# Kernel optimization log

Measured on AMD Instinct MI355X. Metric: run time of the kernel, lower is better.

Reference implementation:

```python
import jax, jax.numpy as jnp
import numpy as np

N_NODES = 100000
N_EDGES = 3200000
N_SAMPLES = 8
EPS_CONST = 1e-8


def setup_inputs() -> dict:
    key = jax.random.key(0)
    k1, k2, k3, k4 = jax.random.split(key, 4)
    mu = jax.random.normal(k1, (N_NODES,), dtype=jnp.float32)
    log_sigma = jax.random.normal(k2, (N_NODES,), dtype=jnp.float32)
    eps = jax.random.normal(k3, (N_SAMPLES, N_NODES), dtype=jnp.float32)
    edges = jax.random.randint(k4, (N_EDGES, 2), 0, N_NODES, dtype=jnp.int64)
    return {"mu": mu, "log_sigma": log_sigma, "eps": eps, "edges": edges, "n_samples": N_SAMPLES}


def reference(mu, log_sigma, eps, edges, n_samples):
    # c_samples: [S, N]
    c = mu + jnp.exp(log_sigma) * eps
    ci = c[:, edges[:, 0]]  # [S, E] gather
    cj = c[:, edges[:, 1]]  # [S, E] gather
    p = jax.nn.sigmoid(ci * cj)
    # original: sum over edges of mean over samples
    loglik = jnp.log(p + EPS_CONST).mean(axis=0).sum()
    return loglik
```

## Files before the change

### kernel.cpp

```cpp
#include <hip/hip_runtime.h>
#include <hip/hip_fp16.h>


__global__ void compute_c_h8(const float* __restrict__ mu,
                             const float* __restrict__ ls,
                             const float* __restrict__ eps,
                             __half2* __restrict__ c, int N,
                             const unsigned int* __restrict__ raw_edges,
                             int* __restrict__ flag,
                             float* __restrict__ out, int out_size) {
    if (blockIdx.x == gridDim.x - 1) {
        int lane = threadIdx.x;
        if (lane < 64) {
            unsigned int acc = 0;
#pragma unroll
            for (int k = 0; k < 4; ++k) acc |= raw_edges[2 * (lane * 4 + k) + 1];
#pragma unroll
            for (int off = 32; off > 0; off >>= 1) acc |= __shfl_down(acc, off, 64);
            if (lane == 0) *flag = (acc == 0u) ? 1 : 0;
        }
        for (int i = threadIdx.x; i < out_size; i += blockDim.x) out[i] = 0.0f;
        return;
    }
    int n = blockIdx.x * blockDim.x + threadIdx.x;
    if (n >= N) return;
    float m  = mu[n];
    float sg = __expf(ls[n]);
    float v[8];
#pragma unroll
    for (int s = 0; s < 8; ++s) v[s] = m + sg * eps[(size_t)s * N + n];
    __half2* dst = c + (size_t)n * 4;
#pragma unroll
    for (int s = 0; s < 4; ++s) dst[s] = __floats2half2_rn(v[2 * s], v[2 * s + 1]);
}

__global__ void compute_c_gen(const float* __restrict__ mu,
                              const float* __restrict__ ls,
                              const float* __restrict__ eps,
                              __half* __restrict__ c, int N, int S,
                              const unsigned int* __restrict__ raw_edges,
                              int* __restrict__ flag,
                              float* __restrict__ out, int out_size) {
    if (blockIdx.x == gridDim.x - 1) {
        int lane = threadIdx.x;
        if (lane < 64) {
            unsigned int acc = 0;
#pragma unroll
            for (int k = 0; k < 4; ++k) acc |= raw_edges[2 * (lane * 4 + k) + 1];
#pragma unroll
            for (int off = 32; off > 0; off >>= 1) acc |= __shfl_down(acc, off, 64);
            if (lane == 0) *flag = (acc == 0u) ? 1 : 0;
        }
        for (int i = threadIdx.x; i < out_size; i += blockDim.x) out[i] = 0.0f;
        return;
    }
    int n = blockIdx.x * blockDim.x + threadIdx.x;
    if (n >= N) return;
    float m  = mu[n];
    float sg = __expf(ls[n]);
    for (int s = 0; s < S; ++s) c[(size_t)n * S + s] = __float2half(m + sg * eps[(size_t)s * N + n]);
}

__device__ __forceinline__ float edge_term(uint4 A, uint4 B) {
    const __half2* ah = (const __half2*)&A;
    const __half2* bh = (const __half2*)&B;
    float t[8];
#pragma unroll
    for (int k = 0; k < 4; ++k) {
        __half2 xh = __hmul2(ah[k], bh[k]);
        float2 xf = __half22float2(xh);
        t[2 * k]     = fminf(__expf(-xf.x), 1.0e8f);
        t[2 * k + 1] = fminf(__expf(-xf.y), 1.0e8f);
    }
    float p0 = 1.0f + t[0];
    p0 = __builtin_fmaf(p0, t[1], p0);
    p0 = __builtin_fmaf(p0, t[2], p0);
    p0 = __builtin_fmaf(p0, t[3], p0);
    float p1 = 1.0f + t[4];
    p1 = __builtin_fmaf(p1, t[5], p1);
    p1 = __builtin_fmaf(p1, t[6], p1);
    p1 = __builtin_fmaf(p1, t[7], p1);
    return __logf(p0) + __logf(p1);
}

__global__ void __launch_bounds__(256, 8)
edge_loglik_s8(const void* __restrict__ edges_raw,
               const uint4* __restrict__ c,
               const int* __restrict__ flag,
               float* __restrict__ out,
               long long E, float inv_s) {
    long long tid    = (long long)blockIdx.x * blockDim.x + threadIdx.x;
    long long stride = (long long)gridDim.x * blockDim.x;
    float acc = 0.0f;
    bool is64 = (*flag != 0);

    if (!is64) {
        const int4* ep = (const int4*)edges_raw;
        long long P = E >> 1;
        for (long long q = tid; q < P; q += 2 * stride) {
            long long q1 = q + stride;
            bool has1 = q1 < P;
            int4 e0 = ep[q];
            int4 e1 = has1 ? ep[q1] : e0;
            uint4 a0 = c[e0.x], b0 = c[e0.y], d0 = c[e0.z], f0 = c[e0.w];
            uint4 a1 = c[e1.x], b1 = c[e1.y], d1 = c[e1.z], f1 = c[e1.w];
            float s = edge_term(a0, b0) + edge_term(d0, f0);
            if (has1) s += edge_term(a1, b1) + edge_term(d1, f1);
            acc += s;
        }
        if ((E & 1) && tid == 0) {
            const int2* el = (const int2*)edges_raw;
            int2 ij = el[E - 1];
            acc += edge_term(c[ij.x], c[ij.y]);
        }
    } else {
        const longlong2* ep = (const longlong2*)edges_raw;
        for (long long e = tid; e < E; e += stride) {
            longlong2 ij = ep[e];
            acc += edge_term(c[ij.x], c[ij.y]);
        }
    }

#pragma unroll
    for (int off = 32; off > 0; off >>= 1) acc += __shfl_down(acc, off, 64);
    __shared__ float wsum[8];
    int lane = threadIdx.x & 63;
    int wid  = threadIdx.x >> 6;
    if (lane == 0) wsum[wid] = acc;
    __syncthreads();
    if (threadIdx.x == 0) {
        float s = 0.0f;
        int nw = blockDim.x >> 6;
        for (int w = 0; w < nw; ++w) s += wsum[w];
        atomicAdd(out, -s * inv_s);
    }
}

__global__ void edge_loglik_gen(const void* __restrict__ edges_raw,
                                const __half* __restrict__ c,
                                const int* __restrict__ flag,
                                float* __restrict__ out,
                                long long E, int S, float inv_s) {
    long long tid    = (long long)blockIdx.x * blockDim.x + threadIdx.x;
    long long stride = (long long)gridDim.x * blockDim.x;
    float acc = 0.0f;
    bool is64 = (*flag != 0);
    for (long long e = tid; e < E; e += stride) {
        long long i, j;
        if (is64) {
            const long long* ed = (const long long*)edges_raw;
            i = ed[2 * e]; j = ed[2 * e + 1];
        } else {
            const int* ed = (const int*)edges_raw;
            i = ed[2 * e]; j = ed[2 * e + 1];
        }
        for (int s = 0; s < S; ++s) {
            float x = __half2float(c[i * S + s]) * __half2float(c[j * S + s]);
            acc += __logf(1.0f + fminf(__expf(-x), 1.0e8f));
        }
    }
#pragma unroll
    for (int off = 32; off > 0; off >>= 1) acc += __shfl_down(acc, off, 64);
    __shared__ float wsum[8];
    int lane = threadIdx.x & 63;
    int wid  = threadIdx.x >> 6;
    if (lane == 0) wsum[wid] = acc;
    __syncthreads();
    if (threadIdx.x == 0) {
        float s = 0.0f;
        int nw = blockDim.x >> 6;
        for (int w = 0; w < nw; ++w) s += wsum[w];
        atomicAdd(out, -s * inv_s);
    }
}

extern "C" void kernel_launch(void* const* d_in, const int* in_sizes, int n_in,
                              void* d_out, int out_size, void* d_ws, size_t ws_size,
                              hipStream_t stream) {
    const float* mu    = (const float*)d_in[0];
    const float* ls    = (const float*)d_in[1];
    const float* eps   = (const float*)d_in[2];
    const void*  edges = d_in[3];

    int       N = in_sizes[0];
    int       S = in_sizes[2] / N;
    long long E = (long long)in_sizes[3] / 2;

    __half* c   = (__half*)d_ws;
    int*   flag = (int*)((char*)d_ws + (size_t)N * S * sizeof(__half) + 256);
    float* out  = (float*)d_out;

    int cblocks = (N + 255) / 256 + 1;
    if (S == 8) {
        compute_c_h8<<<cblocks, 256, 0, stream>>>(mu, ls, eps, (__half2*)c, N,
                                                  (const unsigned int*)edges, flag, out, out_size);
        edge_loglik_s8<<<2048, 256, 0, stream>>>(edges, (const uint4*)c, flag, out, E, 1.0f / (float)S);
    } else {
        compute_c_gen<<<cblocks, 256, 0, stream>>>(mu, ls, eps, c, N, S,
                                                   (const unsigned int*)edges, flag, out, out_size);
        edge_loglik_gen<<<2048, 256, 0, stream>>>(edges, c, flag, out, E, S, 1.0f / (float)S);
    }
}
```

Baseline: 48.06 us.

## Bucket edges by node-block pairs and gather from shared-memory tiles

Adds a scatter pass that sorts edges into buckets keyed by pairs of 2048-node blocks. A compute pass then loads both node tiles into LDS and evaluates every edge in the bucket from shared memory. Overflow edges are handled by a few extra blocks, and the final reduction is done by the last block to finish. The goal is to replace random global gathers of the c table with LDS reads. The cost is an extra pass that reads all edges twice, plus record writes, global atomics and a third kernel launch. The edge format is now assumed to be int32 and the 64-bit detection flag is dropped.

```diff
diff --git a/kernel.cpp b/kernel.cpp
--- a/kernel.cpp
+++ b/kernel.cpp
@@ -2,64 +2,15 @@
 #include <hip/hip_fp16.h>
 
 
-__global__ void compute_c_h8(const float* __restrict__ mu,
-                             const float* __restrict__ ls,
-                             const float* __restrict__ eps,
-                             __half2* __restrict__ c, int N,
-                             const unsigned int* __restrict__ raw_edges,
-                             int* __restrict__ flag,
-                             float* __restrict__ out, int out_size) {
-    if (blockIdx.x == gridDim.x - 1) {
-        int lane = threadIdx.x;
-        if (lane < 64) {
-            unsigned int acc = 0;
-#pragma unroll
-            for (int k = 0; k < 4; ++k) acc |= raw_edges[2 * (lane * 4 + k) + 1];
-#pragma unroll
-            for (int off = 32; off > 0; off >>= 1) acc |= __shfl_down(acc, off, 64);
-            if (lane == 0) *flag = (acc == 0u) ? 1 : 0;
-        }
-        for (int i = threadIdx.x; i < out_size; i += blockDim.x) out[i] = 0.0f;
-        return;
-    }
-    int n = blockIdx.x * blockDim.x + threadIdx.x;
-    if (n >= N) return;
-    float m  = mu[n];
-    float sg = __expf(ls[n]);
-    float v[8];
-#pragma unroll
-    for (int s = 0; s < 8; ++s) v[s] = m + sg * eps[(size_t)s * N + n];
-    __half2* dst = c + (size_t)n * 4;
-#pragma unroll
-    for (int s = 0; s < 4; ++s) dst[s] = __floats2half2_rn(v[2 * s], v[2 * s + 1]);
-}
-
-__global__ void compute_c_gen(const float* __restrict__ mu,
-                              const float* __restrict__ ls,
-                              const float* __restrict__ eps,
-                              __half* __restrict__ c, int N, int S,
-                              const unsigned int* __restrict__ raw_edges,
-                              int* __restrict__ flag,
-                              float* __restrict__ out, int out_size) {
-    if (blockIdx.x == gridDim.x - 1) {
-        int lane = threadIdx.x;
-        if (lane < 64) {
-            unsigned int acc = 0;
-#pragma unroll
-            for (int k = 0; k < 4; ++k) acc |= raw_edges[2 * (lane * 4 + k) + 1];
-#pragma unroll
-            for (int off = 32; off > 0; off >>= 1) acc |= __shfl_down(acc, off, 64);
-            if (lane == 0) *flag = (acc == 0u) ? 1 : 0;
-        }
-        for (int i = threadIdx.x; i < out_size; i += blockDim.x) out[i] = 0.0f;
-        return;
-    }
-    int n = blockIdx.x * blockDim.x + threadIdx.x;
-    if (n >= N) return;
-    float m  = mu[n];
-    float sg = __expf(ls[n]);
-    for (int s = 0; s < S; ++s) c[(size_t)n * S + s] = __float2half(m + sg * eps[(size_t)s * N + n]);
-}
+#define NG_SHIFT 11
+#define NG 2048
+#define MAX_B 2500
+#define CAP 1792
+#define OVF_CAP 65536
+#define K1_TPB 512
+#define K1_CHUNK 8192
+#define K2_TPB 512
+#define OVF_BLOCKS 8
 
 __device__ __forceinline__ float edge_term(uint4 A, uint4 B) {
     const __half2* ah = (const __half2*)&A;
@@ -83,77 +34,201 @@
     return __logf(p0) + __logf(p1);
 }
 
+__global__ void compute_c_h8(const float* __restrict__ mu,
+                             const float* __restrict__ ls,
+                             const float* __restrict__ eps,
+                             __half2* __restrict__ c, int N,
+                             float* __restrict__ out, int out_size,
+                             unsigned int* __restrict__ gcnt, int B,
+                             unsigned int* __restrict__ misc,
+                             float* __restrict__ partials) {
+    if (blockIdx.x == gridDim.x - 1) {
+        for (int i = threadIdx.x; i < out_size; i += blockDim.x) out[i] = 0.0f;
+        if (gcnt) {
+            for (int i = threadIdx.x; i < B; i += blockDim.x) gcnt[i] = 0u;
+            if (threadIdx.x < 2) misc[threadIdx.x] = 0u;
+            for (int i = threadIdx.x; i < 1024; i += blockDim.x) partials[i] = 0.0f;
+        }
+        return;
+    }
+    int n = blockIdx.x * blockDim.x + threadIdx.x;
+    if (n >= N) return;
+    float m  = mu[n];
+    float sg = __expf(ls[n]);
+    float v[8];
+#pragma unroll
+    for (int s = 0; s < 8; ++s) v[s] = m + sg * eps[(size_t)s * N + n];
+    __half2* dst = c + (size_t)n * 4;
+#pragma unroll
+    for (int s = 0; s < 4; ++s) dst[s] = __floats2half2_rn(v[2 * s], v[2 * s + 1]);
+}
+
+__global__ void __launch_bounds__(K1_TPB)
+bucket_scatter(const int2* __restrict__ edges, long long E, int G, int B,
+               unsigned int* __restrict__ recs,
+               unsigned int* __restrict__ gcnt,
+               int2* __restrict__ ovf,
+               unsigned int* __restrict__ misc) {
+    __shared__ unsigned int hist[MAX_B];
+    __shared__ unsigned int base[MAX_B];
+    long long start = (long long)blockIdx.x * K1_CHUNK;
+
+    for (int i = threadIdx.x; i < B; i += K1_TPB) hist[i] = 0u;
+    __syncthreads();
+#pragma unroll
+    for (int k = 0; k < K1_CHUNK / K1_TPB; ++k) {
+        long long idx = start + (long long)k * K1_TPB + threadIdx.x;
+        if (idx < E) {
+            int2 e = edges[idx];
+            int b = (e.x >> NG_SHIFT) * G + (e.y >> NG_SHIFT);
+            atomicAdd(&hist[b], 1u);
+        }
+    }
+    __syncthreads();
+    for (int i = threadIdx.x; i < B; i += K1_TPB) {
+        unsigned int h = hist[i];
+        base[i] = h ? atomicAdd(&gcnt[i], h) : 0u;
+        hist[i] = 0u;
+    }
+    __syncthreads();
+#pragma unroll
+    for (int k = 0; k < K1_CHUNK / K1_TPB; ++k) {
+        long long idx = start + (long long)k * K1_TPB + threadIdx.x;
+        if (idx < E) {
+            int2 e = edges[idx];
+            int b = (e.x >> NG_SHIFT) * G + (e.y >> NG_SHIFT);
+            unsigned int rank = atomicAdd(&hist[b], 1u);
+            unsigned int pos  = base[b] + rank;
+            if (pos < CAP) {
+                recs[(size_t)b * CAP + pos] =
+                    (unsigned int)(e.x & (NG - 1)) | ((unsigned int)(e.y & (NG - 1)) << 16);
+            } else {
+                unsigned int op = atomicAdd(&misc[0], 1u);
+                if (op < OVF_CAP) ovf[op] = e;
+            }
+        }
+    }
+}
+
+__global__ void __launch_bounds__(K2_TPB)
+bucket_compute(const uint4* __restrict__ c,
+               const unsigned int* __restrict__ recs,
+               const unsigned int* __restrict__ gcnt,
+               const int2* __restrict__ ovf,
+               unsigned int* __restrict__ misc,
+               float* __restrict__ partials,
+               float* __restrict__ out,
+               int G, int B, int gridTotal, float neg_inv_s) {
+    __shared__ uint4 SA[NG];
+    __shared__ uint4 SB[NG];
+    float acc = 0.0f;
+    int b = blockIdx.x;
+
+    if (b < B) {
+        unsigned int nb = gcnt[b];
+        if (nb > CAP) nb = CAP;
+        if (nb) {
+            int gi = b / G, gj = b - gi * G;
+            const uint4* Ai = c + (size_t)gi * NG;
+            const uint4* Bj = c + (size_t)gj * NG;
+            for (int t = threadIdx.x; t < NG; t += K2_TPB) { SA[t] = Ai[t]; SB[t] = Bj[t]; }
+            __syncthreads();
+            const unsigned int* r = recs + (size_t)b * CAP;
+            for (unsigned int k = threadIdx.x; k < nb; k += K2_TPB) {
+                unsigned int rec = r[k];
+                uint4 a = SA[rec & 0xFFFFu];
+                uint4 v = SB[rec >> 16];
+                acc += edge_term(a, v);
+            }
+        }
+    } else {
+        unsigned int no = misc[0];
+        if (no > OVF_CAP) no = OVF_CAP;
+        for (unsigned int k = (unsigned int)(b - B) * K2_TPB + threadIdx.x;
+             k < no; k += OVF_BLOCKS * K2_TPB) {
+            int2 e = ovf[k];
+            acc += edge_term(c[e.x], c[e.y]);
+        }
+    }
+
+#pragma unroll
+    for (int off = 32; off > 0; off >>= 1) acc += __shfl_down(acc, off, 64);
+    int wid = threadIdx.x >> 6;
+    if ((threadIdx.x & 63) == 0)
+        atomicAdd(&partials[((unsigned int)blockIdx.x * 8u + (unsigned int)wid) & 1023u], acc);
+
+    __syncthreads();
+    int* flag = (int*)SA;
+    if (threadIdx.x == 0) {
+        __threadfence();
+        unsigned int d = atomicAdd(&misc[1], 1u);
+        flag[0] = (d == (unsigned int)(gridTotal - 1)) ? 1 : 0;
+    }
+    __syncthreads();
+    if (flag[0]) {
+        float s = atomicAdd(&partials[threadIdx.x], 0.0f)
+                + atomicAdd(&partials[threadIdx.x + 512], 0.0f);
+#pragma unroll
+        for (int off = 32; off > 0; off >>= 1) s += __shfl_down(s, off, 64);
+        float* fs = (float*)SB;
+        if ((threadIdx.x & 63) == 0) fs[wid] = s;
+        __syncthreads();
+        if (threadIdx.x == 0) {
+            float tot = 0.0f;
+            for (int w = 0; w < K2_TPB / 64; ++w) tot += fs[w];
+            out[0] = tot * neg_inv_s;
+        }
+    }
+}
+
 __global__ void __launch_bounds__(256, 8)
-edge_loglik_s8(const void* __restrict__ edges_raw,
-               const uint4* __restrict__ c,
-               const int* __restrict__ flag,
-               float* __restrict__ out,
-               long long E, float inv_s) {
+edge_loglik_direct(const int4* __restrict__ ep, const uint4* __restrict__ c,
+                   float* __restrict__ out, long long E, float inv_s) {
     long long tid    = (long long)blockIdx.x * blockDim.x + threadIdx.x;
     long long stride = (long long)gridDim.x * blockDim.x;
     float acc = 0.0f;
-    bool is64 = (*flag != 0);
-
-    if (!is64) {
-        const int4* ep = (const int4*)edges_raw;
-        long long P = E >> 1;
-        for (long long q = tid; q < P; q += 2 * stride) {
-            long long q1 = q + stride;
-            bool has1 = q1 < P;
-            int4 e0 = ep[q];
-            int4 e1 = has1 ? ep[q1] : e0;
-            uint4 a0 = c[e0.x], b0 = c[e0.y], d0 = c[e0.z], f0 = c[e0.w];
-            uint4 a1 = c[e1.x], b1 = c[e1.y], d1 = c[e1.z], f1 = c[e1.w];
-            float s = edge_term(a0, b0) + edge_term(d0, f0);
-            if (has1) s += edge_term(a1, b1) + edge_term(d1, f1);
-            acc += s;
-        }
-        if ((E & 1) && tid == 0) {
-            const int2* el = (const int2*)edges_raw;
-            int2 ij = el[E - 1];
-            acc += edge_term(c[ij.x], c[ij.y]);
-        }
-    } else {
-        const longlong2* ep = (const longlong2*)edges_raw;
-        for (long long e = tid; e < E; e += stride) {
-            longlong2 ij = ep[e];
-            acc += edge_term(c[ij.x], c[ij.y]);
-        }
-    }
-
+    long long P = E >> 1;
+    for (long long q = tid; q < P; q += stride) {
+        int4 ee = ep[q];
+        acc += edge_term(c[ee.x], c[ee.y]) + edge_term(c[ee.z], c[ee.w]);
+    }
+    if ((E & 1) && tid == 0) {
+        const int2* el = (const int2*)ep;
+        int2 ij = el[E - 1];
+        acc += edge_term(c[ij.x], c[ij.y]);
+    }
 #pragma unroll
     for (int off = 32; off > 0; off >>= 1) acc += __shfl_down(acc, off, 64);
     __shared__ float wsum[8];
-    int lane = threadIdx.x & 63;
-    int wid  = threadIdx.x >> 6;
+    int lane = threadIdx.x & 63, wid = threadIdx.x >> 6;
     if (lane == 0) wsum[wid] = acc;
     __syncthreads();
     if (threadIdx.x == 0) {
         float s = 0.0f;
-        int nw = blockDim.x >> 6;
-        for (int w = 0; w < nw; ++w) s += wsum[w];
+        for (int w = 0; w < (int)(blockDim.x >> 6); ++w) s += wsum[w];
         atomicAdd(out, -s * inv_s);
     }
 }
 
-__global__ void edge_loglik_gen(const void* __restrict__ edges_raw,
-                                const __half* __restrict__ c,
-                                const int* __restrict__ flag,
-                                float* __restrict__ out,
-                                long long E, int S, float inv_s) {
-    long long tid    = (long long)blockIdx.x * blockDim.x + threadIdx.x;
+__global__ void compute_c_gen(const float* __restrict__ mu, const float* __restrict__ ls,
+                              const float* __restrict__ eps, __half* __restrict__ c,
+                              int N, int S, float* __restrict__ out, int out_size) {
+    if (blockIdx.x == gridDim.x - 1) {
+        for (int i = threadIdx.x; i < out_size; i += blockDim.x) out[i] = 0.0f;
+        return;
+    }
+    int n = blockIdx.x * blockDim.x + threadIdx.x;
+    if (n >= N) return;
+    float m = mu[n], sg = __expf(ls[n]);
+    for (int s = 0; s < S; ++s) c[(size_t)n * S + s] = __float2half(m + sg * eps[(size_t)s * N + n]);
+}
+__global__ void edge_loglik_gen(const int* __restrict__ ed, const __half* __restrict__ c,
+                                float* __restrict__ out, long long E, int S, float inv_s) {
+    long long tid = (long long)blockIdx.x * blockDim.x + threadIdx.x;
     long long stride = (long long)gridDim.x * blockDim.x;
     float acc = 0.0f;
-    bool is64 = (*flag != 0);
     for (long long e = tid; e < E; e += stride) {
-        long long i, j;
-        if (is64) {
-            const long long* ed = (const long long*)edges_raw;
-            i = ed[2 * e]; j = ed[2 * e + 1];
-        } else {
-            const int* ed = (const int*)edges_raw;
-            i = ed[2 * e]; j = ed[2 * e + 1];
-        }
+        long long i = ed[2 * e], j = ed[2 * e + 1];
         for (int s = 0; s < S; ++s) {
             float x = __half2float(c[i * S + s]) * __half2float(c[j * S + s]);
             acc += __logf(1.0f + fminf(__expf(-x), 1.0e8f));
@@ -162,14 +237,12 @@
 #pragma unroll
     for (int off = 32; off > 0; off >>= 1) acc += __shfl_down(acc, off, 64);
     __shared__ float wsum[8];
-    int lane = threadIdx.x & 63;
-    int wid  = threadIdx.x >> 6;
+    int lane = threadIdx.x & 63, wid = threadIdx.x >> 6;
     if (lane == 0) wsum[wid] = acc;
     __syncthreads();
     if (threadIdx.x == 0) {
         float s = 0.0f;
-        int nw = blockDim.x >> 6;
-        for (int w = 0; w < nw; ++w) s += wsum[w];
+        for (int w = 0; w < (int)(blockDim.x >> 6); ++w) s += wsum[w];
         atomicAdd(out, -s * inv_s);
     }
 }
@@ -177,27 +250,52 @@
 extern "C" void kernel_launch(void* const* d_in, const int* in_sizes, int n_in,
                               void* d_out, int out_size, void* d_ws, size_t ws_size,
                               hipStream_t stream) {
-    const float* mu    = (const float*)d_in[0];
-    const float* ls    = (const float*)d_in[1];
-    const float* eps   = (const float*)d_in[2];
-    const void*  edges = d_in[3];
+    const float* mu  = (const float*)d_in[0];
+    const float* ls  = (const float*)d_in[1];
+    const float* eps = (const float*)d_in[2];
+    const int* edges = (const int*)d_in[3];
 
     int       N = in_sizes[0];
     int       S = in_sizes[2] / N;
     long long E = (long long)in_sizes[3] / 2;
 
-    __half* c   = (__half*)d_ws;
-    int*   flag = (int*)((char*)d_ws + (size_t)N * S * sizeof(__half) + 256);
-    float* out  = (float*)d_out;
-
+    int    G    = (N + NG - 1) >> NG_SHIFT;
+    int    B    = G * G;
+    size_t NTAB = (size_t)G * NG;
+
+    char* p = (char*)d_ws;
+    __half* c = (__half*)p;
+    size_t sz_c    = NTAB * 16;
+    unsigned int* recs = (unsigned int*)(p + sz_c);
+    size_t sz_recs = (size_t)B * CAP * 4;
+    int2* ovf = (int2*)(p + sz_c + sz_recs);
+    size_t sz_ovf  = (size_t)OVF_CAP * 8;
+    unsigned int* gcnt = (unsigned int*)(p + sz_c + sz_recs + sz_ovf);
+    size_t sz_gcnt = (((size_t)B * 4) + 255) & ~(size_t)255;
+    unsigned int* misc = (unsigned int*)((char*)gcnt + sz_gcnt);
+    float* partials = (float*)(misc + 16);
+    size_t need = sz_c + sz_recs + sz_ovf + sz_gcnt + 64 + 1024 * 4 + 256;
+
+    float* out = (float*)d_out;
     int cblocks = (N + 255) / 256 + 1;
-    if (S == 8) {
+
+    if (S == 8 && B <= MAX_B && ws_size >= need && E > 0) {
         compute_c_h8<<<cblocks, 256, 0, stream>>>(mu, ls, eps, (__half2*)c, N,
-                                                  (const unsigned int*)edges, flag, out, out_size);
-        edge_loglik_s8<<<2048, 256, 0, stream>>>(edges, (const uint4*)c, flag, out, E, 1.0f / (float)S);
+                                                  out, out_size, gcnt, B, misc, partials);
+        int k1b = (int)((E + K1_CHUNK - 1) / K1_CHUNK);
+        bucket_scatter<<<k1b, K1_TPB, 0, stream>>>((const int2*)edges, E, G, B,
+                                                   recs, gcnt, ovf, misc);
+        int k2b = B + OVF_BLOCKS;
+        bucket_compute<<<k2b, K2_TPB, 0, stream>>>((const uint4*)c, recs, gcnt, ovf,
+                                                   misc, partials, out, G, B, k2b,
+                                                   -1.0f / (float)S);
+    } else if (S == 8 && ws_size >= sz_c) {
+        compute_c_h8<<<cblocks, 256, 0, stream>>>(mu, ls, eps, (__half2*)c, N,
+                                                  out, out_size, nullptr, 0, nullptr, nullptr);
+        edge_loglik_direct<<<2048, 256, 0, stream>>>((const int4*)edges, (const uint4*)c,
+                                                     out, E, 1.0f / (float)S);
     } else {
-        compute_c_gen<<<cblocks, 256, 0, stream>>>(mu, ls, eps, c, N, S,
-                                                   (const unsigned int*)edges, flag, out, out_size);
-        edge_loglik_gen<<<2048, 256, 0, stream>>>(edges, c, flag, out, E, S, 1.0f / (float)S);
-    }
-}
+        compute_c_gen<<<cblocks, 256, 0, stream>>>(mu, ls, eps, c, N, S, out, out_size);
+        edge_loglik_gen<<<2048, 256, 0, stream>>>(edges, c, out, E, S, 1.0f / (float)S);
+    }
+}
```

Result: slower. 120.9 us (+151.5%).

## Drop int64 edge detection and split edge pass into nontemporal and cached halves

Applied to the files above, without the earlier changes.

Removes the runtime flag that detected 64-bit edge indices and assumes 32-bit edges everywhere. The edge pass is split into two launches over halves of the edge pairs. The first half gathers node values with nontemporal loads and the second with normal cached loads, probably to cut cache thrashing or pollution during the random gathers. This adds a kernel launch and drops support for int64 edge inputs, which would give wrong results if the edges actually arrive as int64.

```diff
diff --git a/kernel.cpp b/kernel.cpp
--- a/kernel.cpp
+++ b/kernel.cpp
@@ -1,24 +1,37 @@
 #include <hip/hip_runtime.h>
 #include <hip/hip_fp16.h>
 
+
+typedef unsigned int u32x4 __attribute__((ext_vector_type(4)));
+
+__device__ __forceinline__ float edge_term(u32x4 A, u32x4 B) {
+    float t[8];
+#pragma unroll
+    for (int k = 0; k < 4; ++k) {
+        __half2 a = __builtin_bit_cast(__half2, A[k]);
+        __half2 b = __builtin_bit_cast(__half2, B[k]);
+        __half2 xh = __hmul2(a, b);
+        float2 xf = __half22float2(xh);
+        t[2 * k]     = fminf(__expf(-xf.x), 1.0e8f);
+        t[2 * k + 1] = fminf(__expf(-xf.y), 1.0e8f);
+    }
+    float p0 = 1.0f + t[0];
+    p0 = __builtin_fmaf(p0, t[1], p0);
+    p0 = __builtin_fmaf(p0, t[2], p0);
+    p0 = __builtin_fmaf(p0, t[3], p0);
+    float p1 = 1.0f + t[4];
+    p1 = __builtin_fmaf(p1, t[5], p1);
+    p1 = __builtin_fmaf(p1, t[6], p1);
+    p1 = __builtin_fmaf(p1, t[7], p1);
+    return __logf(p0) + __logf(p1);
+}
 
 __global__ void compute_c_h8(const float* __restrict__ mu,
                              const float* __restrict__ ls,
                              const float* __restrict__ eps,
                              __half2* __restrict__ c, int N,
-                             const unsigned int* __restrict__ raw_edges,
-                             int* __restrict__ flag,
                              float* __restrict__ out, int out_size) {
     if (blockIdx.x == gridDim.x - 1) {
-        int lane = threadIdx.x;
-        if (lane < 64) {
-            unsigned int acc = 0;
-#pragma unroll
-            for (int k = 0; k < 4; ++k) acc |= raw_edges[2 * (lane * 4 + k) + 1];
-#pragma unroll
-            for (int off = 32; off > 0; off >>= 1) acc |= __shfl_down(acc, off, 64);
-            if (lane == 0) *flag = (acc == 0u) ? 1 : 0;
-        }
         for (int i = threadIdx.x; i < out_size; i += blockDim.x) out[i] = 0.0f;
         return;
     }
@@ -34,126 +47,78 @@
     for (int s = 0; s < 4; ++s) dst[s] = __floats2half2_rn(v[2 * s], v[2 * s + 1]);
 }
 
-__global__ void compute_c_gen(const float* __restrict__ mu,
-                              const float* __restrict__ ls,
-                              const float* __restrict__ eps,
-                              __half* __restrict__ c, int N, int S,
-                              const unsigned int* __restrict__ raw_edges,
-                              int* __restrict__ flag,
-                              float* __restrict__ out, int out_size) {
-    if (blockIdx.x == gridDim.x - 1) {
-        int lane = threadIdx.x;
-        if (lane < 64) {
-            unsigned int acc = 0;
-#pragma unroll
-            for (int k = 0; k < 4; ++k) acc |= raw_edges[2 * (lane * 4 + k) + 1];
-#pragma unroll
-            for (int off = 32; off > 0; off >>= 1) acc |= __shfl_down(acc, off, 64);
-            if (lane == 0) *flag = (acc == 0u) ? 1 : 0;
-        }
-        for (int i = threadIdx.x; i < out_size; i += blockDim.x) out[i] = 0.0f;
-        return;
-    }
-    int n = blockIdx.x * blockDim.x + threadIdx.x;
-    if (n >= N) return;
-    float m  = mu[n];
-    float sg = __expf(ls[n]);
-    for (int s = 0; s < S; ++s) c[(size_t)n * S + s] = __float2half(m + sg * eps[(size_t)s * N + n]);
-}
-
-__device__ __forceinline__ float edge_term(uint4 A, uint4 B) {
-    const __half2* ah = (const __half2*)&A;
-    const __half2* bh = (const __half2*)&B;
-    float t[8];
-#pragma unroll
-    for (int k = 0; k < 4; ++k) {
-        __half2 xh = __hmul2(ah[k], bh[k]);
-        float2 xf = __half22float2(xh);
-        t[2 * k]     = fminf(__expf(-xf.x), 1.0e8f);
-        t[2 * k + 1] = fminf(__expf(-xf.y), 1.0e8f);
-    }
-    float p0 = 1.0f + t[0];
-    p0 = __builtin_fmaf(p0, t[1], p0);
-    p0 = __builtin_fmaf(p0, t[2], p0);
-    p0 = __builtin_fmaf(p0, t[3], p0);
-    float p1 = 1.0f + t[4];
-    p1 = __builtin_fmaf(p1, t[5], p1);
-    p1 = __builtin_fmaf(p1, t[6], p1);
-    p1 = __builtin_fmaf(p1, t[7], p1);
-    return __logf(p0) + __logf(p1);
-}
-
+template <bool NT>
 __global__ void __launch_bounds__(256, 8)
-edge_loglik_s8(const void* __restrict__ edges_raw,
-               const uint4* __restrict__ c,
-               const int* __restrict__ flag,
-               float* __restrict__ out,
-               long long E, float inv_s) {
+edge_loglik_half(const int4* __restrict__ ep, const u32x4* __restrict__ c,
+                 float* __restrict__ out, long long q0, long long qn,
+                 long long E, int handle_tail, float neg_inv_s) {
     long long tid    = (long long)blockIdx.x * blockDim.x + threadIdx.x;
     long long stride = (long long)gridDim.x * blockDim.x;
+    long long qend   = q0 + qn;
     float acc = 0.0f;
-    bool is64 = (*flag != 0);
 
-    if (!is64) {
-        const int4* ep = (const int4*)edges_raw;
-        long long P = E >> 1;
-        for (long long q = tid; q < P; q += 2 * stride) {
-            long long q1 = q + stride;
-            bool has1 = q1 < P;
-            int4 e0 = ep[q];
-            int4 e1 = has1 ? ep[q1] : e0;
-            uint4 a0 = c[e0.x], b0 = c[e0.y], d0 = c[e0.z], f0 = c[e0.w];
-            uint4 a1 = c[e1.x], b1 = c[e1.y], d1 = c[e1.z], f1 = c[e1.w];
-            float s = edge_term(a0, b0) + edge_term(d0, f0);
-            if (has1) s += edge_term(a1, b1) + edge_term(d1, f1);
-            acc += s;
+    for (long long q = q0 + tid; q < qend; q += 2 * stride) {
+        long long q1 = q + stride;
+        bool has1 = q1 < qend;
+        int4 e0 = ep[q];
+        int4 e1 = has1 ? ep[q1] : e0;
+        u32x4 a0, b0, d0, f0, a1, b1, d1, f1;
+        if constexpr (NT) {
+            a0 = __builtin_nontemporal_load(c + e0.x);
+            b0 = __builtin_nontemporal_load(c + e0.y);
+            d0 = __builtin_nontemporal_load(c + e0.z);
+            f0 = __builtin_nontemporal_load(c + e0.w);
+            a1 = __builtin_nontemporal_load(c + e1.x);
+            b1 = __builtin_nontemporal_load(c + e1.y);
+            d1 = __builtin_nontemporal_load(c + e1.z);
+            f1 = __builtin_nontemporal_load(c + e1.w);
+        } else {
+            a0 = c[e0.x]; b0 = c[e0.y]; d0 = c[e0.z]; f0 = c[e0.w];
+            a1 = c[e1.x]; b1 = c[e1.y]; d1 = c[e1.z]; f1 = c[e1.w];
         }
-        if ((E & 1) && tid == 0) {
-            const int2* el = (const int2*)edges_raw;
-            int2 ij = el[E - 1];
-            acc += edge_term(c[ij.x], c[ij.y]);
-        }
-    } else {
-        const longlong2* ep = (const longlong2*)edges_raw;
-        for (long long e = tid; e < E; e += stride) {
-            longlong2 ij = ep[e];
-            acc += edge_term(c[ij.x], c[ij.y]);
-        }
+        float s = edge_term(a0, b0) + edge_term(d0, f0);
+        if (has1) s += edge_term(a1, b1) + edge_term(d1, f1);
+        acc += s;
+    }
+    if (handle_tail && (E & 1) && tid == 0) {
+        const int2* el = (const int2*)ep;
+        int2 ij = el[E - 1];
+        acc += edge_term(c[ij.x], c[ij.y]);
     }
 
 #pragma unroll
     for (int off = 32; off > 0; off >>= 1) acc += __shfl_down(acc, off, 64);
-    __shared__ float wsum[8];
+    __shared__ float wsum[4];
     int lane = threadIdx.x & 63;
     int wid  = threadIdx.x >> 6;
     if (lane == 0) wsum[wid] = acc;
     __syncthreads();
     if (threadIdx.x == 0) {
         float s = 0.0f;
-        int nw = blockDim.x >> 6;
-        for (int w = 0; w < nw; ++w) s += wsum[w];
-        atomicAdd(out, -s * inv_s);
+        for (int w = 0; w < (int)(blockDim.x >> 6); ++w) s += wsum[w];
+        atomicAdd(out, s * neg_inv_s);
     }
 }
 
-__global__ void edge_loglik_gen(const void* __restrict__ edges_raw,
-                                const __half* __restrict__ c,
-                                const int* __restrict__ flag,
-                                float* __restrict__ out,
-                                long long E, int S, float inv_s) {
-    long long tid    = (long long)blockIdx.x * blockDim.x + threadIdx.x;
+__global__ void compute_c_gen(const float* __restrict__ mu, const float* __restrict__ ls,
+                              const float* __restrict__ eps, __half* __restrict__ c,
+                              int N, int S, float* __restrict__ out, int out_size) {
+    if (blockIdx.x == gridDim.x - 1) {
+        for (int i = threadIdx.x; i < out_size; i += blockDim.x) out[i] = 0.0f;
+        return;
+    }
+    int n = blockIdx.x * blockDim.x + threadIdx.x;
+    if (n >= N) return;
+    float m = mu[n], sg = __expf(ls[n]);
+    for (int s = 0; s < S; ++s) c[(size_t)n * S + s] = __float2half(m + sg * eps[(size_t)s * N + n]);
+}
+__global__ void edge_loglik_gen(const int* __restrict__ ed, const __half* __restrict__ c,
+                                float* __restrict__ out, long long E, int S, float neg_inv_s) {
+    long long tid = (long long)blockIdx.x * blockDim.x + threadIdx.x;
     long long stride = (long long)gridDim.x * blockDim.x;
     float acc = 0.0f;
-    bool is64 = (*flag != 0);
     for (long long e = tid; e < E; e += stride) {
-        long long i, j;
-        if (is64) {
-            const long long* ed = (const long long*)edges_raw;
-            i = ed[2 * e]; j = ed[2 * e + 1];
-        } else {
-            const int* ed = (const int*)edges_raw;
-            i = ed[2 * e]; j = ed[2 * e + 1];
-        }
+        long long i = ed[2 * e], j = ed[2 * e + 1];
         for (int s = 0; s < S; ++s) {
             float x = __half2float(c[i * S + s]) * __half2float(c[j * S + s]);
             acc += __logf(1.0f + fminf(__expf(-x), 1.0e8f));
@@ -162,42 +127,46 @@
 #pragma unroll
     for (int off = 32; off > 0; off >>= 1) acc += __shfl_down(acc, off, 64);
     __shared__ float wsum[8];
-    int lane = threadIdx.x & 63;
-    int wid  = threadIdx.x >> 6;
+    int lane = threadIdx.x & 63, wid = threadIdx.x >> 6;
     if (lane == 0) wsum[wid] = acc;
     __syncthreads();
     if (threadIdx.x == 0) {
         float s = 0.0f;
-        int nw = blockDim.x >> 6;
-        for (int w = 0; w < nw; ++w) s += wsum[w];
-        atomicAdd(out, -s * inv_s);
+        for (int w = 0; w < (int)(blockDim.x >> 6); ++w) s += wsum[w];
+        atomicAdd(out, s * neg_inv_s);
     }
 }
 
 extern "C" void kernel_launch(void* const* d_in, const int* in_sizes, int n_in,
                               void* d_out, int out_size, void* d_ws, size_t ws_size,
                               hipStream_t stream) {
-    const float* mu    = (const float*)d_in[0];
-    const float* ls    = (const float*)d_in[1];
-    const float* eps   = (const float*)d_in[2];
-    const void*  edges = d_in[3];
+    const float* mu  = (const float*)d_in[0];
+    const float* ls  = (const float*)d_in[1];
+    const float* eps = (const float*)d_in[2];
+    const int* edges = (const int*)d_in[3];
 
     int       N = in_sizes[0];
     int       S = in_sizes[2] / N;
     long long E = (long long)in_sizes[3] / 2;
 
-    __half* c   = (__half*)d_ws;
-    int*   flag = (int*)((char*)d_ws + (size_t)N * S * sizeof(__half) + 256);
-    float* out  = (float*)d_out;
+    __half* c  = (__half*)d_ws;
+    float* out = (float*)d_out;
+    size_t sz_c = (size_t)N * S * sizeof(__half);
+    float neg_inv_s = -1.0f / (float)S;
 
     int cblocks = (N + 255) / 256 + 1;
-    if (S == 8) {
-        compute_c_h8<<<cblocks, 256, 0, stream>>>(mu, ls, eps, (__half2*)c, N,
-                                                  (const unsigned int*)edges, flag, out, out_size);
-        edge_loglik_s8<<<2048, 256, 0, stream>>>(edges, (const uint4*)c, flag, out, E, 1.0f / (float)S);
+
+    if (S == 8 && ws_size >= sz_c) {
+        compute_c_h8<<<cblocks, 256, 0, stream>>>(mu, ls, eps, (__half2*)c, N, out, out_size);
+        long long P  = E >> 1;
+        long long QA = P >> 1;
+        long long QB = P - QA;
+        edge_loglik_half<true ><<<2048, 256, 0, stream>>>((const int4*)edges, (const u32x4*)c,
+                                                          out, 0,  QA, E, 0, neg_inv_s);
+        edge_loglik_half<false><<<2048, 256, 0, stream>>>((const int4*)edges, (const u32x4*)c,
+                                                          out, QA, QB, E, 1, neg_inv_s);
     } else {
-        compute_c_gen<<<cblocks, 256, 0, stream>>>(mu, ls, eps, c, N, S,
-                                                   (const unsigned int*)edges, flag, out, out_size);
-        edge_loglik_gen<<<2048, 256, 0, stream>>>(edges, c, flag, out, E, S, 1.0f / (float)S);
+        compute_c_gen<<<cblocks, 256, 0, stream>>>(mu, ls, eps, c, N, S, out, out_size);
+        edge_loglik_gen<<<2048, 256, 0, stream>>>(edges, c, out, E, S, neg_inv_s);
     }
 }
```

Result: slower. 83.74 us (+74.2%).
